# Optimization experiments

Hardware: AMD Instinct MI355X
Metric: run time of the kernel (lower is better)

The kernel has to match this reference:

```python
import jax, jax.numpy as jnp
import numpy as np

B, N, C = 16, 2048, 3           # images, proposals/image, classes (incl. background)
K = 100                         # num_detections kept per class
SCORE_THRESH = 0.05
NMS_THRESH = 0.5
MIN_ANGLE = 10.0                # process_box min width (self.min_angle)
WX, WW = 1.0, 1.0               # box_coder reg_weights
NEG = jnp.float32(-1e9)


def setup_inputs() -> dict:
    key = jax.random.key(0)
    k1, k2, k3, k4 = jax.random.split(key, 4)
    class_logit = jax.random.normal(k1, (B, N, C), jnp.float32)
    box_regression = jax.random.normal(k2, (B, N, 2 * C), jnp.float32) * 0.1
    starts = jax.random.uniform(k3, (B, N), dtype=jnp.float32) * 300.0
    widths = jax.random.uniform(k4, (B, N), dtype=jnp.float32) * 50.0 + 12.0
    proposal = jnp.stack([starts, starts + widths], axis=-1)  # [B,N,2] 1-D intervals
    return {"class_logit": class_logit, "box_regression": box_regression,
            "proposal": proposal, "image_shape": 360}


def _decode(delta, prop):
    w = prop[:, 1] - prop[:, 0]
    ctr = prop[:, 0] + 0.5 * w
    dx = delta[:, 0] / WX
    dw = jnp.minimum(delta[:, 1] / WW, 4.0)  # clamp like torchvision
    pc = dx * w + ctr
    pw = jnp.exp(dw) * w
    return jnp.stack([pc - 0.5 * pw, pc + 0.5 * pw], axis=-1)  # [N,2]


def _iou_1d(a, b):
    inter = jnp.maximum(0.0, jnp.minimum(a[:, None, 1], b[None, :, 1])
                        - jnp.maximum(a[:, None, 0], b[None, :, 0]))
    union = (a[:, None, 1] - a[:, None, 0]) + (b[None, :, 1] - b[None, :, 0]) - inter
    return inter / jnp.maximum(union, 1e-8)  # [Na,Nb]


def _infer_one_class(score, delta, prop, image_shape):
    # score [N], delta [N,2], prop [N,2] -> [K,3] (start, end, score); invalid slots score=NEG
    box = _decode(delta, prop)
    lo = jnp.clip(box[:, 0], 0.0, image_shape)
    hi = jnp.clip(box[:, 1], 0.0, image_shape)
    box = jnp.stack([lo, hi], axis=-1)
    valid = ((hi - lo) >= MIN_ANGLE) & (score >= SCORE_THRESH)
    ms = jnp.where(valid, score, NEG)
    order = jnp.argsort(-ms)
    b = box[order]
    s = ms[order]
    sup = jax.lax.stop_gradient(_iou_1d(b, b)) > NMS_THRESH  # [N,N] bool
    idx = jnp.arange(N)

    def body(keep, i):  # greedy NMS in score order
        kill = sup[i] & keep[i] & (idx > i)
        return keep & ~kill, None

    keep0 = s > 0.5 * NEG
    keep, _ = jax.lax.scan(body, keep0, idx)
    ks = jnp.where(keep, s, NEG)
    top_s, top_i = jax.lax.top_k(ks, K)
    top_b = b[top_i]
    return jnp.concatenate([top_b, top_s[:, None]], axis=-1)  # [K,3]


def reference(class_logit, box_regression, proposal, image_shape):
    img = jnp.float32(image_shape)
    scores = jax.nn.softmax(class_logit, axis=-1)[..., 1:]        # [B,N,C-1] fg classes
    deltas = box_regression.reshape(B, N, C, 2)[:, :, 1:]         # [B,N,C-1,2]
    scores = jnp.moveaxis(scores, -1, 1)                          # [B,C-1,N]
    deltas = jnp.moveaxis(deltas, 2, 1)                           # [B,C-1,N,2]
    f = jax.vmap(jax.vmap(_infer_one_class, in_axes=(0, 0, None, None)),
                 in_axes=(0, 0, 0, None))
    return f(scores, deltas, proposal, img)  # [B, C-1, K, 3]
```

## Files before the change

kernel.cpp:

```cpp
#include <hip/hip_runtime.h>
#include <math.h>

#define B_IMG 16
#define N_PROP 2048
#define C_CLS 3
#define K_OUT 100
#define NTHREADS 1024
#define NWAVES (NTHREADS / 64)
#define NBLK64 (N_PROP / 64)


__device__ __forceinline__ unsigned long long shfl_xor_u64(unsigned long long v, int lx) {
    unsigned int lo = (unsigned int)__shfl_xor((int)(unsigned int)(v & 0xffffffffull), lx, 64);
    unsigned int hi = (unsigned int)__shfl_xor((int)(unsigned int)(v >> 32), lx, 64);
    return ((unsigned long long)hi << 32) | (unsigned long long)lo;
}
__device__ __forceinline__ float readlane_f(float v, int l) {
    return __int_as_float(__builtin_amdgcn_readlane(__float_as_int(v), l));
}
__device__ __forceinline__ unsigned long long readlane_u64(unsigned long long v, int l) {
    unsigned int lo = (unsigned int)__builtin_amdgcn_readlane((int)(unsigned int)(v & 0xffffffffull), l);
    unsigned int hi = (unsigned int)__builtin_amdgcn_readlane((int)(unsigned int)(v >> 32), l);
    return ((unsigned long long)hi << 32) | (unsigned long long)lo;
}
__device__ __forceinline__ bool iou_gt_half(float inter, float uni) {
    float b = fmaxf(uni, 1e-8f);
    float lhs = 2.0f * inter;
    if (__builtin_expect(lhs > b, 0)) {
        if (lhs > b * 0x1.000004p0f) return true;
        double bb = (double)b;
        return (double)inter * 2.0 > bb * 0x1.000001p0;
    }
    return false;
}
__device__ __forceinline__ float parse_imgf(int raw) {
    return (raw > 0 && raw < 1000000) ? (float)raw : __int_as_float(raw);
}

__global__ __launch_bounds__(NTHREADS)
void roiheads_fused(const float* __restrict__ class_logit,
                    const float* __restrict__ box_reg,
                    const float* __restrict__ proposal,
                    const int* __restrict__ image_shape_p,
                    float* __restrict__ out)
{
#pragma clang fp contract(off)
    __shared__ unsigned long long skey[N_PROP];
    __shared__ float blo_n[N_PROP], bhi_n[N_PROP];
    __shared__ float slo[N_PROP], shi[N_PROP];
    __shared__ unsigned char keep[N_PROP];
    __shared__ unsigned short alv[2][N_PROP];
    __shared__ float2 cbox[64];
    __shared__ unsigned long long sup[64];
    __shared__ unsigned long long kmask[NBLK64];
    __shared__ int wsum[NWAVES];
    __shared__ int sh_nvalid;

    const int tid = threadIdx.x;
    const int lane = tid & 63;
    const int wid = tid >> 6;
    const int img = blockIdx.x >> 1;
    const int cls = blockIdx.x & 1;
    const float imgf = parse_imgf(image_shape_p[0]);

    if (tid == 0) sh_nvalid = 0;

    const int p0 = (wid << 7) | (lane << 1);
    const int p1 = p0 | 1;
    const unsigned long long below = (1ull << lane) - 1ull;

    unsigned long long r0 = 0, r1 = 0;
#pragma unroll
    for (int e = 0; e < 2; ++e) {
        const int n = p0 + e;
        const size_t g = (size_t)img * N_PROP + n;
        const float* lg = class_logit + g * C_CLS;
        float l0 = lg[0], l1 = lg[1], l2 = lg[2];
        float mx = fmaxf(l0, fmaxf(l1, l2));
        float e0 = (float)exp((double)(l0 - mx));
        float e1 = (float)exp((double)(l1 - mx));
        float e2 = (float)exp((double)(l2 - mx));
        float denom = (e0 + e1) + e2;
        float score = ((cls == 0) ? e1 : e2) / denom;

        const float* dr = box_reg + g * (2 * C_CLS) + 2 * (cls + 1);
        float dx = dr[0];
        float dw = fminf(dr[1], 4.0f);
        const float* pp = proposal + g * 2;
        float pA = pp[0], pB = pp[1];
        float w = pB - pA;
        float ctr = pA + 0.5f * w;
        float tt = dx * w;
        float pc = tt + ctr;
        float pw = (float)exp((double)dw) * w;
        float half = 0.5f * pw;
        float lo = pc - half;
        float hi = pc + half;
        lo = fminf(fmaxf(lo, 0.0f), imgf);
        hi = fminf(fmaxf(hi, 0.0f), imgf);
        bool valid = ((hi - lo) >= 10.0f) && (score >= 0.05f);
        float ms = valid ? score : -1e9f;
        blo_n[n] = lo;
        bhi_n[n] = hi;
        unsigned int uu = __float_as_uint(ms);
        unsigned int enc = (uu & 0x80000000u) ? ~uu : (uu | 0x80000000u);
        unsigned long long key = ((unsigned long long)enc << 32) |
                                 (unsigned long long)(0xFFFFFFFFu - (unsigned int)n);
        if (e == 0) r0 = key; else r1 = key;
    }

    auto pass_inreg = [&](int k, int j) {
        if (j == 1) {
            bool desc = ((p0 & k) == 0);
            bool sw = desc ? (r0 < r1) : (r0 > r1);
            if (sw) { unsigned long long t = r0; r0 = r1; r1 = t; }
        } else {
            int lx = j >> 1;
            unsigned long long o0 = shfl_xor_u64(r0, lx);
            unsigned long long o1 = shfl_xor_u64(r1, lx);
            bool desc = ((p0 & k) == 0);
            bool lower = ((p0 & j) == 0);
            bool takeMax = (lower == desc);
            r0 = takeMax ? (r0 > o0 ? r0 : o0) : (r0 < o0 ? r0 : o0);
            r1 = takeMax ? (r1 > o1 ? r1 : o1) : (r1 < o1 ? r1 : o1);
        }
    };

    for (int k = 2; k <= 128; k <<= 1)
        for (int j = k >> 1; j >= 1; j >>= 1)
            pass_inreg(k, j);

    for (int k = 256; k <= N_PROP; k <<= 1) {
        skey[p0] = r0; skey[p1] = r1;
        __syncthreads();
        for (int j = k >> 1; j >= 128; j >>= 1) {
            int i = ((tid & ~(j - 1)) << 1) | (tid & (j - 1));
            int part = i | j;
            unsigned long long a = skey[i], b = skey[part];
            bool desc_blk = ((i & k) == 0);
            bool sw = desc_blk ? (a < b) : (a > b);
            if (sw) { skey[i] = b; skey[part] = a; }
            __syncthreads();
        }
        r0 = skey[p0]; r1 = skey[p1];
        for (int j = 64; j >= 1; j >>= 1)
            pass_inreg(k, j);
    }
    skey[p0] = r0; skey[p1] = r1;
    __syncthreads();

    for (int i = tid; i < N_PROP; i += NTHREADS) {
        unsigned long long kk = skey[i];
        unsigned int e = (unsigned int)(kk >> 32);
        unsigned int sb = (e & 0x80000000u) ? (e & 0x7FFFFFFFu) : ~e;
        float s = __uint_as_float(sb);
        unsigned int n = 0xFFFFFFFFu - (unsigned int)(kk & 0xFFFFFFFFull);
        slo[i] = blo_n[n];
        shi[i] = bhi_n[n];
        keep[i] = 0;
        bool v = (s > -5e8f);
        unsigned long long mb = __ballot(v);
        if (lane == 0) atomicAdd(&sh_nvalid, __popcll(mb));
        alv[0][i] = (unsigned short)i;
    }
    __syncthreads();

    int na = sh_nvalid;
    int cur = 0;
    int tk = 0;

    while (na > 0) {
        const int m = (na < 64) ? na : 64;

        unsigned short cp = alv[cur][lane];
        bool cin = (lane < m);
        float qloc = cin ? slo[cp] : 0.0f;
        float qhic = cin ? shi[cp] : 0.0f;

#pragma unroll
        for (int rr4 = 0; rr4 < 4; ++rr4) {
            int rr = (wid << 2) | rr4;
            unsigned long long row = 0;
            if (rr < m) {
                unsigned short rp = alv[cur][rr];
                float rlo = slo[rp], rhi = shi[rp];
                float inter = fmaxf(fminf(rhi, qhic) - fmaxf(rlo, qloc), 0.0f);
                float uni = (rhi - rlo) + (qhic - qloc) - inter;
                bool kill = cin && (lane > rr) && iou_gt_half(inter, uni);
                row = __ballot(kill);
            }
            if (lane == 0) sup[rr] = row;
        }

        const int iA = 64 + tid;
        const int iB = 64 + NTHREADS + tid;
        const bool vA = (iA < na);
        const bool vB = (iB < na);
        unsigned short qqA = vA ? alv[cur][iA] : 0;
        unsigned short qqB = vB ? alv[cur][iB] : 0;
        float qAlo = vA ? slo[qqA] : 0.0f;
        float qAhi = vA ? shi[qqA] : 0.0f;
        float qBlo = vB ? slo[qqB] : 0.0f;
        float qBhi = vB ? shi[qqB] : 0.0f;
        __syncthreads();

        unsigned long long rw = sup[lane];
        unsigned long long A = (m >= 64) ? ~0ull : ((1ull << m) - 1ull);
        unsigned long long kept = 0;
        while (A) {
            int c = __builtin_ctzll(A);
            kept |= (1ull << c);
            A &= ~(readlane_u64(rw, c) | (1ull << c));
        }
        const int cnt = __popcll(kept);

        if (wid == 0) {
            bool alive = cin && ((kept >> lane) & 1ull);
            if (alive) {
                keep[cp] = 1;
                int rank = __popcll(kept & below);
                cbox[rank] = make_float2(qloc, qhic);
            }
        }
        __syncthreads();
        tk += cnt;
        if (tk >= K_OUT) break;

        bool survA = vA, survB = vB;
        {
            float qAw = qAhi - qAlo;
            float qBw = qBhi - qBlo;
            bool dA = false, dB = false;
#pragma unroll 4
            for (int r = 0; r < cnt; ++r) {
                float2 cb = cbox[r];
                float interA = fmaxf(fminf(qAhi, cb.y) - fmaxf(qAlo, cb.x), 0.0f);
                float uniA = qAw + (cb.y - cb.x) - interA;
                dA |= iou_gt_half(interA, uniA);
                float interB = fmaxf(fminf(qBhi, cb.y) - fmaxf(qBlo, cb.x), 0.0f);
                float uniB = qBw + (cb.y - cb.x) - interB;
                dB |= iou_gt_half(interB, uniB);
            }
            survA = vA && !dA;
            survB = vB && !dB;
        }
        unsigned long long mbA = __ballot(survA);
        unsigned long long mbB = __ballot(survB);
        if (lane == 0) wsum[wid] = (__popcll(mbA) << 16) | __popcll(mbB);
        __syncthreads();
        int offA = 0, offB = 0, totA = 0, totB = 0;
#pragma unroll
        for (int w2 = 0; w2 < NWAVES; ++w2) {
            unsigned pk = (unsigned)wsum[w2];
            int ca = (int)(pk >> 16), cb2 = (int)(pk & 0xffffu);
            if (w2 < wid) { offA += ca; offB += cb2; }
            totA += ca; totB += cb2;
        }
        if (survA) alv[cur ^ 1][offA + __popcll(mbA & below)] = qqA;
        if (survB) alv[cur ^ 1][totA + offB + __popcll(mbB & below)] = qqB;
        __syncthreads();
        na = totA + totB;
        cur ^= 1;
    }

    for (int blk = wid; blk < NBLK64; blk += NWAVES) {
        bool kk = keep[blk * 64 + lane] != 0;
        unsigned long long mb = __ballot(kk);
        if (lane == 0) kmask[blk] = mb;
    }
    __syncthreads();
    {
        float* outp = out + (((size_t)img * 2 + cls) * K_OUT) * 3;
        for (int blk = wid; blk < NBLK64; blk += NWAVES) {
            int kc = 0, nc = 0, nk = 0;
            for (int b = 0; b < NBLK64; ++b) {
                int pc = __popcll(kmask[b]);
                nk += pc;
                if (b < blk) { kc += pc; nc += 64 - pc; }
            }
            if (kc >= K_OUT && nk + nc >= K_OUT && nc >= K_OUT) continue;
            int p = blk * 64 + lane;
            unsigned long long mb = kmask[blk];
            bool k = (mb >> lane) & 1ull;
            int rk = kc + __popcll(mb & below);
            int rn = nc + __popcll((~mb) & below);
            if (k) {
                if (rk < K_OUT) {
                    unsigned long long kk2 = skey[p];
                    unsigned int e = (unsigned int)(kk2 >> 32);
                    unsigned int sb = (e & 0x80000000u) ? (e & 0x7FFFFFFFu) : ~e;
                    outp[rk * 3 + 0] = slo[p];
                    outp[rk * 3 + 1] = shi[p];
                    outp[rk * 3 + 2] = __uint_as_float(sb);
                }
            } else {
                int oi = nk + rn;
                if (oi < K_OUT) {
                    outp[oi * 3 + 0] = slo[p];
                    outp[oi * 3 + 1] = shi[p];
                    outp[oi * 3 + 2] = -1e9f;
                }
            }
        }
    }
}

extern "C" void kernel_launch(void* const* d_in, const int* in_sizes, int n_in,
                              void* d_out, int out_size, void* d_ws, size_t ws_size,
                              hipStream_t stream) {
    const float* class_logit = (const float*)d_in[0];
    const float* box_reg     = (const float*)d_in[1];
    const float* prop        = (const float*)d_in[2];
    const int*   image_shape = (const int*)d_in[3];
    float* out = (float*)d_out;
    (void)d_ws; (void)ws_size;

    roiheads_fused<<<dim3(B_IMG * 2), dim3(NTHREADS), 0, stream>>>(
        class_logit, box_reg, prop, image_shape, out);
}
```

Before: 109.5 us.

## Fuse greedy candidate NMS with tail suppression per wave, drop shared sup matrix

Every wave now redundantly runs the serial greedy scan over the 64-candidate chunk, computing each row's IoU kills on the fly with readlane and ballot instead of building a shared suppression matrix. The same pass tests the tail boxes against each newly kept candidate. This removes the sup/cbox shared buffers and two block-wide barriers per iteration. In exchange the serial loop does more work per step, and the IoU test now always takes the double-precision path instead of a cheap float pre-check.

Measured after the change: 103.6 us. 1.06x faster.

```diff
diff --git a/kernel.cpp b/kernel.cpp
--- a/kernel.cpp
+++ b/kernel.cpp
@@ -18,20 +18,9 @@
 __device__ __forceinline__ float readlane_f(float v, int l) {
     return __int_as_float(__builtin_amdgcn_readlane(__float_as_int(v), l));
 }
-__device__ __forceinline__ unsigned long long readlane_u64(unsigned long long v, int l) {
-    unsigned int lo = (unsigned int)__builtin_amdgcn_readlane((int)(unsigned int)(v & 0xffffffffull), l);
-    unsigned int hi = (unsigned int)__builtin_amdgcn_readlane((int)(unsigned int)(v >> 32), l);
-    return ((unsigned long long)hi << 32) | (unsigned long long)lo;
-}
 __device__ __forceinline__ bool iou_gt_half(float inter, float uni) {
-    float b = fmaxf(uni, 1e-8f);
-    float lhs = 2.0f * inter;
-    if (__builtin_expect(lhs > b, 0)) {
-        if (lhs > b * 0x1.000004p0f) return true;
-        double bb = (double)b;
-        return (double)inter * 2.0 > bb * 0x1.000001p0;
-    }
-    return false;
+    double b = (double)fmaxf(uni, 1e-8f);
+    return (double)inter * 2.0 > b * 0x1.000001p0;
 }
 __device__ __forceinline__ float parse_imgf(int raw) {
     return (raw > 0 && raw < 1000000) ? (float)raw : __int_as_float(raw);
@@ -50,8 +39,6 @@
     __shared__ float slo[N_PROP], shi[N_PROP];
     __shared__ unsigned char keep[N_PROP];
     __shared__ unsigned short alv[2][N_PROP];
-    __shared__ float2 cbox[64];
-    __shared__ unsigned long long sup[64];
     __shared__ unsigned long long kmask[NBLK64];
     __shared__ int wsum[NWAVES];
     __shared__ int sh_nvalid;
@@ -177,21 +164,6 @@
         float qloc = cin ? slo[cp] : 0.0f;
         float qhic = cin ? shi[cp] : 0.0f;
 
-#pragma unroll
-        for (int rr4 = 0; rr4 < 4; ++rr4) {
-            int rr = (wid << 2) | rr4;
-            unsigned long long row = 0;
-            if (rr < m) {
-                unsigned short rp = alv[cur][rr];
-                float rlo = slo[rp], rhi = shi[rp];
-                float inter = fmaxf(fminf(rhi, qhic) - fmaxf(rlo, qloc), 0.0f);
-                float uni = (rhi - rlo) + (qhic - qloc) - inter;
-                bool kill = cin && (lane > rr) && iou_gt_half(inter, uni);
-                row = __ballot(kill);
-            }
-            if (lane == 0) sup[rr] = row;
-        }
-
         const int iA = 64 + tid;
         const int iB = 64 + NTHREADS + tid;
         const bool vA = (iA < na);
@@ -202,51 +174,43 @@
         float qAhi = vA ? shi[qqA] : 0.0f;
         float qBlo = vB ? slo[qqB] : 0.0f;
         float qBhi = vB ? shi[qqB] : 0.0f;
-        __syncthreads();
-
-        unsigned long long rw = sup[lane];
+        const float qAw = qAhi - qAlo;
+        const float qBw = qBhi - qBlo;
+
         unsigned long long A = (m >= 64) ? ~0ull : ((1ull << m) - 1ull);
         unsigned long long kept = 0;
+        bool deadA = false, deadB = false;
         while (A) {
             int c = __builtin_ctzll(A);
-            kept |= (1ull << c);
-            A &= ~(readlane_u64(rw, c) | (1ull << c));
+            unsigned long long bit = 1ull << c;
+            kept |= bit;
+            float cl = readlane_f(qloc, c);
+            float ch = readlane_f(qhic, c);
+            float cw = ch - cl;
+            float inter = fmaxf(fminf(ch, qhic) - fmaxf(cl, qloc), 0.0f);
+            float uni = cw + (qhic - qloc) - inter;
+            bool kill = (lane > c) && iou_gt_half(inter, uni);
+            float inA = fmaxf(fminf(qAhi, ch) - fmaxf(qAlo, cl), 0.0f);
+            float unA = qAw + cw - inA;
+            deadA |= iou_gt_half(inA, unA);
+            float inB = fmaxf(fminf(qBhi, ch) - fmaxf(qBlo, cl), 0.0f);
+            float unB = qBw + cw - inB;
+            deadB |= iou_gt_half(inB, unB);
+            A &= ~(__ballot(kill) | bit);
         }
         const int cnt = __popcll(kept);
 
         if (wid == 0) {
-            bool alive = cin && ((kept >> lane) & 1ull);
-            if (alive) {
-                keep[cp] = 1;
-                int rank = __popcll(kept & below);
-                cbox[rank] = make_float2(qloc, qhic);
-            }
-        }
-        __syncthreads();
+            if (cin && ((kept >> lane) & 1ull)) keep[cp] = 1;
+        }
         tk += cnt;
         if (tk >= K_OUT) break;
 
-        bool survA = vA, survB = vB;
-        {
-            float qAw = qAhi - qAlo;
-            float qBw = qBhi - qBlo;
-            bool dA = false, dB = false;
-#pragma unroll 4
-            for (int r = 0; r < cnt; ++r) {
-                float2 cb = cbox[r];
-                float interA = fmaxf(fminf(qAhi, cb.y) - fmaxf(qAlo, cb.x), 0.0f);
-                float uniA = qAw + (cb.y - cb.x) - interA;
-                dA |= iou_gt_half(interA, uniA);
-                float interB = fmaxf(fminf(qBhi, cb.y) - fmaxf(qBlo, cb.x), 0.0f);
-                float uniB = qBw + (cb.y - cb.x) - interB;
-                dB |= iou_gt_half(interB, uniB);
-            }
-            survA = vA && !dA;
-            survB = vB && !dB;
-        }
+        bool survA = vA && !deadA;
+        bool survB = vB && !deadB;
         unsigned long long mbA = __ballot(survA);
         unsigned long long mbB = __ballot(survB);
-        if (lane == 0) wsum[wid] = (__popcll(mbA) << 16) | __popcll(mbB);
+        if (lane == 0) wsum[wid] = (__popcll(mbA) << 16) | (int)__popcll(mbB);
         __syncthreads();
         int offA = 0, offB = 0, totA = 0, totB = 0;
 #pragma unroll
@@ -262,6 +226,7 @@
         na = totA + totB;
         cur ^= 1;
     }
+    __syncthreads();
 
     for (int blk = wid; blk < NBLK64; blk += NWAVES) {
         bool kk = keep[blk * 64 + lane] != 0;
```
